# Optimization experiments

Hardware: AMD Instinct MI355X
Metric: run time of the kernel (lower is better)

Reference implementation:

```python
import jax, jax.numpy as jnp
import numpy as np

L, B, H, N2 = 2048, 16, 256, 32  # seq len, batch, d_model, d_state/2 (conjugate pairs)
EPS = 1e-5


def setup_inputs() -> dict:
    key = jax.random.key(0)
    ks = jax.random.split(key, 12)
    rn = lambda k, s, sc=1.0: sc * jax.random.normal(k, s, jnp.float32)
    x = rn(ks[0], (L, B, H))
    # S4 (SSSD) parameterization
    log_dt = jnp.log(0.001) + jax.random.uniform(ks[1], (H,), jnp.float32) * (np.log(0.1) - np.log(0.001))
    w_log_real = jnp.full((H, N2), np.log(0.5), jnp.float32)
    w_imag = jnp.pi * jnp.broadcast_to(jnp.arange(N2, dtype=jnp.float32), (H, N2))
    P_re, P_im = rn(ks[2], (1, H, N2), 0.1), rn(ks[3], (1, H, N2), 0.1)   # rank-1 low-rank term
    B_re, B_im = rn(ks[4], (1, H, N2), 0.5), rn(ks[5], (1, H, N2), 0.5)
    C_re, C_im = rn(ks[6], (2, H, N2), 0.5), rn(ks[7], (2, H, N2), 0.5)   # 2 channels (bidirectional)
    D = rn(ks[8], (1, H))
    Wout = rn(ks[9], (2 * H, H), 1.0 / np.sqrt(H))  # output linear -> GLU
    bout = jnp.zeros((2 * H,), jnp.float32)
    gamma = jnp.ones((H,), jnp.float32)
    beta = jnp.zeros((H,), jnp.float32)
    return dict(x=x, log_dt=log_dt, w_log_real=w_log_real, w_imag=w_imag,
                P_re=P_re, P_im=P_im, B_re=B_re, B_im=B_im, C_re=C_re, C_im=C_im,
                D=D, Wout=Wout, bout=bout, gamma=gamma, beta=beta)


def _s4_layer(x, log_dt, w_log_real, w_imag, P_re, P_im, B_re, B_im, C_re, C_im,
              D, Wout, bout, gamma, beta):
    u = jnp.transpose(x, (1, 2, 0))  # (B, H, L)
    Lx = u.shape[-1]
    # ---- SSKernelNPLR kernel generation (Cauchy resolvent + rank-1 Woodbury) ----
    dt = jnp.exp(log_dt)                               # (H,)
    w = -jnp.exp(w_log_real) + 1j * w_imag             # (H, N2)
    Bc = B_re + 1j * B_im                              # (1, H, N2)
    Cc = C_re + 1j * C_im                              # (2, H, N2)
    Pc = P_re + 1j * P_im                              # (1, H, N2)
    Bt = jnp.concatenate([Bc, Pc], axis=0)             # (2, H, N2)
    Ct = jnp.concatenate([Cc, jnp.conj(Pc)], axis=0)   # (3, H, N2)
    Fh = Lx // 2 + 1
    omega = jnp.exp(-2j * jnp.pi * jnp.arange(Fh) / Lx).astype(jnp.complex64)
    z = 2.0 * (1.0 - omega) / (1.0 + omega)            # bilinear-transform nodes
    wd = w * dt[:, None].astype(w.dtype)               # dt folded into A
    v = Bt[:, None, :, :] * Ct[None, :, :, :]          # (2, 3, H, N2)
    inv1 = 1.0 / (z[None, :, None] - wd[:, None, :])                 # (H, Fh, N2)
    inv2 = 1.0 / (z[None, :, None] - jnp.conj(wd)[:, None, :])
    # cauchy with conjugate-pair symmetry
    r = jnp.einsum('abhn,hfn->abhf', v, inv1) + jnp.einsum('abhn,hfn->abhf', jnp.conj(v), inv2)
    r = r * dt[None, None, :, None].astype(r.dtype)    # (2, 3, H, Fh)
    # rank-1 Woodbury correction
    k_f = r[:-1, :-1] - r[:-1, -1:] * r[-1:, :-1] / (1.0 + r[-1:, -1:])  # (1, 2, H, Fh)
    k_f = k_f * 2.0 / (1.0 + omega)
    k = jnp.fft.irfft(k_f, n=Lx, axis=-1)[0]           # (2, H, L) real kernel, 2 = fwd/bwd
    # ---- bidirectional FFT convolution ----
    kk = jnp.pad(k[0], ((0, 0), (0, Lx))) + jnp.pad(k[1][:, ::-1], ((0, 0), (Lx, 0)))  # (H, 2L)
    kf = jnp.fft.rfft(kk, n=2 * Lx)                    # (H, L+1)
    uf = jnp.fft.rfft(u, n=2 * Lx)                     # (B, H, L+1)
    y = jnp.fft.irfft(uf * kf[None], n=2 * Lx)[..., :Lx]  # (B, H, L)
    y = y + u * D[0][None, :, None]                    # skip connection D
    y = jax.nn.gelu(y, approximate=False)
    y2 = jnp.einsum('dh,bhl->bdl', Wout, y) + bout[None, :, None]  # (B, 2H, L)
    y = y2[:, :H] * jax.nn.sigmoid(y2[:, H:])          # GLU over channel dim
    # ---- wrapper: residual + permute back + LayerNorm ----
    xo = jnp.transpose(y + u, (2, 0, 1))               # (L, B, H)
    mu = jnp.mean(xo, axis=-1, keepdims=True)
    var = jnp.mean(jnp.square(xo - mu), axis=-1, keepdims=True)
    return (xo - mu) * jax.lax.rsqrt(var + EPS) * gamma + beta


def reference(x, log_dt, w_log_real, w_imag, P_re, P_im, B_re, B_im, C_re, C_im,
              D, Wout, bout, gamma, beta):
    return _s4_layer(x, log_dt, w_log_real, w_imag, P_re, P_im, B_re, B_im,
                     C_re, C_im, D, Wout, bout, gamma, beta)
```

## Files before the change

kernel.cpp:

```cpp
#include <hip/hip_runtime.h>


#define PI_F 3.14159265358979323846f
#define LP(i) ((i) + ((i) >> 4))

typedef __attribute__((ext_vector_type(8))) short bf16x8;
typedef __attribute__((ext_vector_type(4))) float f32x4;

__device__ __forceinline__ float2 cmulf(float2 a, float2 b) {
    return make_float2(a.x*b.x - a.y*b.y, a.x*b.y + a.y*b.x);
}
__device__ __forceinline__ unsigned short f2bf(float f) {
    unsigned int u = __float_as_uint(f);
    u += 0x7fffu + ((u >> 16) & 1u);
    return (unsigned short)(u >> 16);
}

template<int SGN>
__device__ __forceinline__ void fft16(float2 v[16]) {
    float2 tsw;
#define SW(i,j) { tsw = v[i]; v[i] = v[j]; v[j] = tsw; }
    SW(1,8) SW(2,4) SW(3,12) SW(5,10) SW(7,14) SW(11,13)
#undef SW
    const float C8[8] = {1.f, 0.92387953251f, 0.70710678119f, 0.38268343236f,
                         0.f, -0.38268343236f, -0.70710678119f, -0.92387953251f};
    const float S8[8] = {0.f, 0.38268343236f, 0.70710678119f, 0.92387953251f,
                         1.f, 0.92387953251f, 0.70710678119f, 0.38268343236f};
    #pragma unroll
    for (int s = 0; s < 4; ++s) {
        const int Ns = 1 << s;
        #pragma unroll
        for (int j = 0; j < 8; ++j) {
            const int k  = j & (Ns - 1);
            const int i0 = ((j >> s) << (s + 1)) | k;
            const int i1 = i0 + Ns;
            const int ti = k << (3 - s);
            const float cs = C8[ti];
            const float sn = (SGN < 0) ? -S8[ti] : S8[ti];
            float2 a = v[i0], b = v[i1];
            float2 t = make_float2(cs*b.x - sn*b.y, cs*b.y + sn*b.x);
            v[i0] = make_float2(a.x + t.x, a.y + t.y);
            v[i1] = make_float2(a.x - t.x, a.y - t.y);
        }
    }
}

template<int SGN>
__device__ __forceinline__ void fft4096p(float2 v[16], float2* lds, int t) {
    fft16<SGN>(v);
    float s1, c1;
    __sincosf((float)SGN * (2.0f * PI_F / 4096.0f) * (float)t, &s1, &c1);
    float2 w1 = make_float2(c1, s1), cur = make_float2(1.f, 0.f);
    #pragma unroll
    for (int k = 1; k < 16; ++k) { cur = cmulf(cur, w1); v[k] = cmulf(v[k], cur); }
    __syncthreads();
    #pragma unroll
    for (int k = 0; k < 16; ++k) lds[t * 17 + k] = v[k];
    __syncthreads();
    const int k1 = t & 15, m2 = t >> 4;
    #pragma unroll
    for (int m1 = 0; m1 < 16; ++m1) v[m1] = lds[(m1 * 16 + m2) * 17 + k1];
    fft16<SGN>(v);
    float s2, c2;
    __sincosf((float)SGN * (2.0f * PI_F / 256.0f) * (float)m2, &s2, &c2);
    float2 w2 = make_float2(c2, s2); cur = make_float2(1.f, 0.f);
    #pragma unroll
    for (int j = 1; j < 16; ++j) { cur = cmulf(cur, w2); v[j] = cmulf(v[j], cur); }
    __syncthreads();
    #pragma unroll
    for (int j = 0; j < 16; ++j) lds[m2 * 273 + j * 17 + k1] = v[j];
    __syncthreads();
    #pragma unroll
    for (int m = 0; m < 16; ++m) v[m] = lds[m * 273 + (t >> 4) * 17 + k1];
    fft16<SGN>(v);
}

template<int SGN>
__device__ __forceinline__ void fft_fused(float2* A, int N, int logN,
                                          int tid, int nthr) {
    __syncthreads();
    for (int j = tid; j < N; j += nthr) {
        int r = (int)(__brev((unsigned)j) >> (32 - logN));
        if (r > j) { float2 t = A[LP(j)]; A[LP(j)] = A[LP(r)]; A[LP(r)] = t; }
    }
    __syncthreads();
    int s = 0;
    if (logN & 1) {
        for (int j = tid; j < (N >> 1); j += nthr) {
            int i0 = 2 * j;
            float2 a = A[LP(i0)], b = A[LP(i0 + 1)];
            A[LP(i0)]     = make_float2(a.x + b.x, a.y + b.y);
            A[LP(i0 + 1)] = make_float2(a.x - b.x, a.y - b.y);
        }
        __syncthreads();
        s = 1;
    }
    for (; s < logN; s += 2) {
        const int Ns = 1 << s;
        for (int g = tid; g < (N >> 2); g += nthr) {
            int k = g & (Ns - 1);
            int base = ((g >> s) << (s + 2)) | k;
            float2 a0 = A[LP(base)];
            float2 a1 = A[LP(base + Ns)];
            float2 a2 = A[LP(base + 2*Ns)];
            float2 a3 = A[LP(base + 3*Ns)];
            float ang1 = (float)SGN * PI_F * (float)k / (float)Ns;
            float sn1, cs1; __sincosf(ang1, &sn1, &cs1);
            float2 t = make_float2(cs1*a1.x - sn1*a1.y, cs1*a1.y + sn1*a1.x);
            float2 b0 = make_float2(a0.x + t.x, a0.y + t.y);
            float2 b1 = make_float2(a0.x - t.x, a0.y - t.y);
            t = make_float2(cs1*a3.x - sn1*a3.y, cs1*a3.y + sn1*a3.x);
            float2 b2 = make_float2(a2.x + t.x, a2.y + t.y);
            float2 b3 = make_float2(a2.x - t.x, a2.y - t.y);
            float ang2 = (float)SGN * PI_F * (float)k / (float)(2 * Ns);
            float sn2, cs2; __sincosf(ang2, &sn2, &cs2);
            t = make_float2(cs2*b2.x - sn2*b2.y, cs2*b2.y + sn2*b2.x);
            A[LP(base)]        = make_float2(b0.x + t.x, b0.y + t.y);
            A[LP(base + 2*Ns)] = make_float2(b0.x - t.x, b0.y - t.y);
            float c2p, s2p;
            if (SGN < 0) { c2p = sn2; s2p = -cs2; } else { c2p = -sn2; s2p = cs2; }
            t = make_float2(c2p*b3.x - s2p*b3.y, c2p*b3.y + s2p*b3.x);
            A[LP(base + Ns)]   = make_float2(b1.x + t.x, b1.y + t.y);
            A[LP(base + 3*Ns)] = make_float2(b1.x - t.x, b1.y - t.y);
        }
        __syncthreads();
    }
}

__global__ void k0_convW(const float* __restrict__ W, unsigned short* __restrict__ Wb)
{
    int i = blockIdx.x * 256 + threadIdx.x;
    if (i < 512 * 256) Wb[i] = f2bf(W[i]);
}

__global__ __launch_bounds__(256) void k1_kergen(const float* __restrict__ log_dt,
                          const float* __restrict__ wlr, const float* __restrict__ wim,
                          const float* __restrict__ Pre, const float* __restrict__ Pim,
                          const float* __restrict__ Bre, const float* __restrict__ Bim,
                          const float* __restrict__ Cre, const float* __restrict__ Cim,
                          float2* __restrict__ kf_out)
{
    __shared__ float4 T0[32], T1[32], T2[32], T3[32];
    int h = blockIdx.x;
    int tid = threadIdx.x;
    float dt = expf(log_dt[h]);
    if (tid < 32) {
        int i = h * 32 + tid;
        float wre = -expf(wlr[i]) * dt;
        float wi  = wim[i] * dt;
        float2 B  = make_float2(Bre[i], Bim[i]);
        float2 P  = make_float2(Pre[i], Pim[i]);
        float2 C0 = make_float2(Cre[i], Cim[i]);
        float2 C1 = make_float2(Cre[8192 + i], Cim[8192 + i]);
        float2 Pc = make_float2(P.x, -P.y);
        float2 v00 = cmulf(B, C0), v01 = cmulf(B, C1), v02 = cmulf(B, Pc);
        float2 v10 = cmulf(P, C0), v11 = cmulf(P, C1), v12 = cmulf(P, Pc);
        T0[tid] = make_float4(wre, wi, v00.x, v00.y);
        T1[tid] = make_float4(v01.x, v01.y, v02.x, v02.y);
        T2[tid] = make_float4(v10.x, v10.y, v11.x, v11.y);
        T3[tid] = make_float4(v12.x, v12.y, 0.f, 0.f);
    }
    __syncthreads();
    int f = blockIdx.y * 256 + tid;
    if (f > 1024) return;
    float ang = -(2.0f * PI_F / 2048.0f) * (float)f;
    float sn, cs;
    sincosf(ang, &sn, &cs);
    float2 onep = make_float2(1.0f + cs, sn);
    float invo = __builtin_amdgcn_rcpf(onep.x * onep.x + onep.y * onep.y);
    float2 oinv = make_float2(onep.x * invo, -onep.y * invo);
    float2 z = cmulf(make_float2(2.0f * (1.0f - cs), -2.0f * sn), oinv);
    float2 r00 = {0,0}, r01 = {0,0}, r02 = {0,0};
    float2 r10 = {0,0}, r11 = {0,0}, r12 = {0,0};
    #pragma unroll 4
    for (int n = 0; n < 32; ++n) {
        float4 a  = T0[n];
        float4 bq = T1[n];
        float4 cq = T2[n];
        float4 dq = T3[n];
        float zx  = z.x - a.x;
        float d1y = z.y - a.y;
        float d2y = z.y + a.y;
        float inv1 = __builtin_amdgcn_rcpf(zx * zx + d1y * d1y);
        float inv2 = __builtin_amdgcn_rcpf(zx * zx + d2y * d2y);
        float sx = zx * (inv1 + inv2);
        float dx = zx * (inv1 - inv2);
        float sy = -(d1y * inv1 + d2y * inv2);
        float dy = d1y * inv1 - d2y * inv2;
        r00.x += a.z*sx + a.w*dy;  r00.y += a.z*sy + a.w*dx;
        r01.x += bq.x*sx + bq.y*dy; r01.y += bq.x*sy + bq.y*dx;
        r02.x += bq.z*sx + bq.w*dy; r02.y += bq.z*sy + bq.w*dx;
        r10.x += cq.x*sx + cq.y*dy; r10.y += cq.x*sy + cq.y*dx;
        r11.x += cq.z*sx + cq.w*dy; r11.y += cq.z*sy + cq.w*dx;
        r12.x += dq.x*sx + dq.y*dy; r12.y += dq.x*sy + dq.y*dx;
    }
    r00.x *= dt; r00.y *= dt; r01.x *= dt; r01.y *= dt; r02.x *= dt; r02.y *= dt;
    r10.x *= dt; r10.y *= dt; r11.x *= dt; r11.y *= dt; r12.x *= dt; r12.y *= dt;
    float2 den = make_float2(1.0f + r12.x, r12.y);
    float invd = __builtin_amdgcn_rcpf(den.x * den.x + den.y * den.y);
    float2 idn = make_float2(den.x * invd, -den.y * invd);
    float2 fac = make_float2(2.0f * oinv.x, 2.0f * oinv.y);
    float2 t0 = cmulf(cmulf(r02, r10), idn);
    float2 k0 = cmulf(make_float2(r00.x - t0.x, r00.y - t0.y), fac);
    float2 t1 = cmulf(cmulf(r02, r11), idn);
    float2 k1 = cmulf(make_float2(r01.x - t1.x, r01.y - t1.y), fac);
    kf_out[(size_t)h * 1025 + f]         = k0;
    kf_out[(size_t)(256 + h) * 1025 + f] = k1;
}

__global__ __launch_bounds__(256) void k2_kernelfft(const float2* __restrict__ kfin,
                                                    float2* __restrict__ kfout)
{
    __shared__ float2 A2[2176];
    __shared__ float2 A4[4352];
    int h = blockIdx.x, tid = threadIdx.x;
    const float2* s0 = kfin + (size_t)h * 1025;
    const float2* s1 = kfin + (size_t)(256 + h) * 1025;
    for (int j = tid; j < 2048; j += 256) {
        float2 q0, q1;
        if (j == 0)          { q0 = s0[0];    q0.y = 0.0f; q1 = s1[0];    q1.y = 0.0f; }
        else if (j < 1024)   { q0 = s0[j];                 q1 = s1[j]; }
        else if (j == 1024)  { q0 = s0[1024]; q0.y = 0.0f; q1 = s1[1024]; q1.y = 0.0f; }
        else { float2 t0 = s0[2048 - j], t1 = s1[2048 - j];
               q0 = make_float2(t0.x, -t0.y); q1 = make_float2(t1.x, -t1.y); }
        A2[LP(j)] = make_float2(q0.x - q1.y, q0.y + q1.x);
    }
    fft_fused<+1>(A2, 2048, 11, tid, 256);
    const float scl = 1.0f / 2048.0f;
    for (int j = tid; j < 2048; j += 256) {
        float2 v = A2[LP(j)];
        A4[LP(j)]        = make_float2(v.x * scl, 0.0f);
        A4[LP(4095 - j)] = make_float2(v.y * scl, 0.0f);
    }
    fft_fused<-1>(A4, 4096, 12, tid, 256);
    for (int F = tid; F <= 2048; F += 256)
        kfout[(size_t)h * 2049 + F] = A4[LP(F)];
}

__global__ void k3_transpose(const float* __restrict__ x, float* __restrict__ u)
{
    __shared__ float tile[32][33];
    int p0 = blockIdx.x * 32;
    int l0 = blockIdx.y * 32;
    int tx = threadIdx.x, ty = threadIdx.y;
    for (int i = ty; i < 32; i += 8)
        tile[i][tx] = x[(size_t)(l0 + i) * 4096 + p0 + tx];
    __syncthreads();
    for (int i = ty; i < 32; i += 8)
        u[(size_t)(p0 + i) * 2048 + l0 + tx] = tile[tx][i];
}

__global__ __launch_bounds__(256) void k4_conv(const float* __restrict__ u,
        const float2* __restrict__ kf, const float* __restrict__ Dp,
        unsigned short* __restrict__ ygb)
{
    __shared__ float2 lds[4366];
    int h  = blockIdx.x & 255;
    int bp = blockIdx.x >> 8;
    int t  = threadIdx.x;
    const float* u0 = u + (size_t)((2*bp)   * 256 + h) * 2048;
    const float* u1 = u + (size_t)((2*bp+1) * 256 + h) * 2048;
    float2 v[16], us[8];
    #pragma unroll
    for (int n1 = 0; n1 < 8; ++n1) {
        int j = n1 * 256 + t;
        us[n1] = make_float2(u0[j], u1[j]);
        v[n1] = us[n1];
        v[n1 + 8] = make_float2(0.f, 0.f);
    }
    fft4096p<-1>(v, lds, t);
    const float2* kfh = kf + (size_t)h * 2049;
    #pragma unroll
    for (int j2 = 0; j2 < 16; ++j2) {
        int f = t + 256 * j2;
        float2 K;
        if (f <= 2048) K = kfh[f];
        else { float2 q = kfh[4096 - f]; K = make_float2(q.x, -q.y); }
        v[j2] = cmulf(v[j2], K);
    }
    fft4096p<+1>(v, lds, t);
    float d = Dp[h];
    unsigned short* o0 = ygb + (size_t)((2*bp)   * 256 + h) * 2048;
    unsigned short* o1 = ygb + (size_t)((2*bp+1) * 256 + h) * 2048;
    const float iscl = 1.0f / 4096.0f;
    #pragma unroll
    for (int j2 = 0; j2 < 8; ++j2) {
        int l = t + 256 * j2;
        float y0 = v[j2].x * iscl + d * us[j2].x;
        float y1 = v[j2].y * iscl + d * us[j2].y;
        o0[l] = f2bf(0.5f * y0 * (1.0f + erff(y0 * 0.70710678118654752f)));
        o1[l] = f2bf(0.5f * y1 * (1.0f + erff(y1 * 0.70710678118654752f)));
    }
}

__global__ __launch_bounds__(256, 2) void k56_gemm_glu_ln(const unsigned short* __restrict__ ygb,
        const unsigned short* __restrict__ Wb, const float* __restrict__ bout,
        const float* __restrict__ u, const float* __restrict__ gamma,
        const float* __restrict__ beta, float* __restrict__ out)
{
    __shared__ short yt[64][264];
    __shared__ short Wl[64][264];
    __shared__ float bo[512];
    __shared__ float gb2[512];
    int b  = blockIdx.y;
    int l0 = blockIdx.x * 64;
    int tid = threadIdx.x;
    int lane = tid & 63, w = tid >> 6;
    int cc = lane & 15, gg = lane >> 4;
    bo[tid] = bout[tid]; bo[tid + 256] = bout[tid + 256];
    gb2[tid] = gamma[tid]; gb2[tid + 256] = beta[tid];
    int li = tid & 63;
    #pragma unroll 4
    for (int it = 0; it < 64; ++it) {
        int hh = (tid >> 6) + it * 4;
        yt[li][hh] = (short)ygb[(size_t)(b * 256 + hh) * 2048 + l0 + li];
    }
    __syncthreads();
    const short* brow = &yt[16 * w + cc][0];
    bf16x8 bfr[8];
    #pragma unroll
    for (int ks = 0; ks < 8; ++ks) bfr[ks] = *(const bf16x8*)(brow + ks * 32 + gg * 8);
    f32x4 acc[32];
    #pragma unroll
    for (int tt = 0; tt < 32; ++tt) acc[tt] = (f32x4){0.f, 0.f, 0.f, 0.f};
    const int fr = tid >> 5, fch = tid & 31;
    bf16x8 pre[8];
    #pragma unroll
    for (int j = 0; j < 8; ++j)
        pre[j] = *(const bf16x8*)(Wb + (size_t)(fr + j * 8) * 256 + fch * 8);
    #pragma unroll
    for (int c = 0; c < 8; ++c) {
        #pragma unroll
        for (int j = 0; j < 8; ++j)
            *(bf16x8*)&Wl[fr + j * 8][fch * 8] = pre[j];
        __syncthreads();
        if (c < 7) {
            #pragma unroll
            for (int j = 0; j < 8; ++j)
                pre[j] = *(const bf16x8*)(Wb + (size_t)((c + 1) * 64 + fr + j * 8) * 256 + fch * 8);
        }
        #pragma unroll
        for (int ks = 0; ks < 8; ++ks) {
            #pragma unroll
            for (int tl = 0; tl < 4; ++tl) {
                bf16x8 afrag = *(const bf16x8*)&Wl[tl * 16 + cc][ks * 32 + gg * 8];
                acc[c * 4 + tl] = __builtin_amdgcn_mfma_f32_16x16x32_bf16(
                    afrag, bfr[ks], acc[c * 4 + tl], 0, 0, 0);
            }
        }
        __syncthreads();
    }
    int l = l0 + 16 * w + cc;
    const float* up = u + (size_t)b * 256 * 2048 + l;
    float s = 0.f, q2 = 0.f;
    #pragma unroll
    for (int tt = 0; tt < 16; ++tt) {
        #pragma unroll
        for (int r = 0; r < 4; ++r) {
            int P = tt * 16 + gg * 4 + r;
            float ya = acc[tt][r] + bo[P];
            float gb = acc[tt + 16][r] + bo[256 + P];
            float gv = ya / (1.0f + expf(-gb));
            float val = gv + up[(size_t)P * 2048];
            acc[tt][r] = val;
            s += val; q2 += val * val;
        }
    }
    s  += __shfl_xor(s, 16);  s  += __shfl_xor(s, 32);
    q2 += __shfl_xor(q2, 16); q2 += __shfl_xor(q2, 32);
    float mu = s * (1.0f / 256.0f);
    float var = q2 * (1.0f / 256.0f) - mu * mu;
    float rstd = rsqrtf(var + 1e-5f);
    float* ob = out + (size_t)(l * 16 + b) * 256;
    #pragma unroll
    for (int tt = 0; tt < 16; ++tt) {
        int P0 = tt * 16 + gg * 4;
        float4 o4;
        o4.x = (acc[tt][0] - mu) * rstd * gb2[P0 + 0] + gb2[256 + P0 + 0];
        o4.y = (acc[tt][1] - mu) * rstd * gb2[P0 + 1] + gb2[256 + P0 + 1];
        o4.z = (acc[tt][2] - mu) * rstd * gb2[P0 + 2] + gb2[256 + P0 + 2];
        o4.w = (acc[tt][3] - mu) * rstd * gb2[P0 + 3] + gb2[256 + P0 + 3];
        *(float4*)(ob + P0) = o4;
    }
}

extern "C" void kernel_launch(void* const* d_in, const int* in_sizes, int n_in,
                              void* d_out, int out_size, void* d_ws, size_t ws_size,
                              hipStream_t stream)
{
    (void)in_sizes; (void)n_in; (void)out_size; (void)ws_size;
    const float* x      = (const float*)d_in[0];
    const float* log_dt = (const float*)d_in[1];
    const float* wlr    = (const float*)d_in[2];
    const float* wim    = (const float*)d_in[3];
    const float* Pre    = (const float*)d_in[4];
    const float* Pim    = (const float*)d_in[5];
    const float* Bre    = (const float*)d_in[6];
    const float* Bim    = (const float*)d_in[7];
    const float* Cre    = (const float*)d_in[8];
    const float* Cim    = (const float*)d_in[9];
    const float* Dp     = (const float*)d_in[10];
    const float* Wout   = (const float*)d_in[11];
    const float* bout   = (const float*)d_in[12];
    const float* gamma  = (const float*)d_in[13];
    const float* beta   = (const float*)d_in[14];

    float* ws  = (float*)d_ws;
    float* u   = ws;
    unsigned short* ygb = (unsigned short*)(ws + 8388608);
    char*  ob  = (char*)d_out;
    float2* kF  = (float2*)(ob);
    float2* kfo = (float2*)(ob + 4198400);
    unsigned short* Wb = (unsigned short*)(ob + 8394752);

    k0_convW<<<dim3(512), 256, 0, stream>>>(Wout, Wb);
    k1_kergen<<<dim3(256, 5), 256, 0, stream>>>(log_dt, wlr, wim, Pre, Pim, Bre, Bim, Cre, Cim, kF);
    k2_kernelfft<<<dim3(256), 256, 0, stream>>>(kF, kfo);
    k3_transpose<<<dim3(128, 64), dim3(32, 8), 0, stream>>>(x, u);
    k4_conv<<<dim3(2048), 256, 0, stream>>>(u, kfo, Dp, ygb);
    k56_gemm_glu_ln<<<dim3(32, 16), 256, 0, stream>>>(ygb, Wb, bout, u, gamma, beta, (float*)d_out);
}
```

Before: 130.7 us.

## Widen kernel-FFT blocks, raise conv occupancy, stage residual in LDS for GLU+LN

Launches the kernel-FFT stage with 1024 threads per block instead of 256, adds a min-blocks hint of 4 to the conv kernel's launch bounds, and in the GEMM/GLU/LayerNorm kernel loads the residual tile into shared memory (aliasing the yt/Wl buffers) with coalesced reads. Before, each thread read the residual with a stride of 2048 floats. The changes target latency in the small-grid FFT and uncoalesced global reads in the epilogue. The occupancy hint may force register spills in the conv kernel, and the extra LDS pass adds a sync.

```diff
diff --git a/kernel.cpp b/kernel.cpp
--- a/kernel.cpp
+++ b/kernel.cpp
@@ -208,15 +208,16 @@
     kf_out[(size_t)(256 + h) * 1025 + f] = k1;
 }
 
-__global__ __launch_bounds__(256) void k2_kernelfft(const float2* __restrict__ kfin,
-                                                    float2* __restrict__ kfout)
+__global__ __launch_bounds__(1024) void k2_kernelfft(const float2* __restrict__ kfin,
+                                                     float2* __restrict__ kfout)
 {
     __shared__ float2 A2[2176];
     __shared__ float2 A4[4352];
     int h = blockIdx.x, tid = threadIdx.x;
+    const int NT = 1024;
     const float2* s0 = kfin + (size_t)h * 1025;
     const float2* s1 = kfin + (size_t)(256 + h) * 1025;
-    for (int j = tid; j < 2048; j += 256) {
+    for (int j = tid; j < 2048; j += NT) {
         float2 q0, q1;
         if (j == 0)          { q0 = s0[0];    q0.y = 0.0f; q1 = s1[0];    q1.y = 0.0f; }
         else if (j < 1024)   { q0 = s0[j];                 q1 = s1[j]; }
@@ -225,15 +226,15 @@
                q0 = make_float2(t0.x, -t0.y); q1 = make_float2(t1.x, -t1.y); }
         A2[LP(j)] = make_float2(q0.x - q1.y, q0.y + q1.x);
     }
-    fft_fused<+1>(A2, 2048, 11, tid, 256);
+    fft_fused<+1>(A2, 2048, 11, tid, NT);
     const float scl = 1.0f / 2048.0f;
-    for (int j = tid; j < 2048; j += 256) {
+    for (int j = tid; j < 2048; j += NT) {
         float2 v = A2[LP(j)];
         A4[LP(j)]        = make_float2(v.x * scl, 0.0f);
         A4[LP(4095 - j)] = make_float2(v.y * scl, 0.0f);
     }
-    fft_fused<-1>(A4, 4096, 12, tid, 256);
-    for (int F = tid; F <= 2048; F += 256)
+    fft_fused<-1>(A4, 4096, 12, tid, NT);
+    for (int F = tid; F <= 2048; F += NT)
         kfout[(size_t)h * 2049 + F] = A4[LP(F)];
 }
 
@@ -250,7 +251,7 @@
         u[(size_t)(p0 + i) * 2048 + l0 + tx] = tile[tx][i];
 }
 
-__global__ __launch_bounds__(256) void k4_conv(const float* __restrict__ u,
+__global__ __launch_bounds__(256, 4) void k4_conv(const float* __restrict__ u,
         const float2* __restrict__ kf, const float* __restrict__ Dp,
         unsigned short* __restrict__ ygb)
 {
@@ -298,8 +299,10 @@
         const float* __restrict__ u, const float* __restrict__ gamma,
         const float* __restrict__ beta, float* __restrict__ out)
 {
-    __shared__ short yt[64][264];
-    __shared__ short Wl[64][264];
+    __shared__ __align__(16) char smem[67584];
+    short (*yt)[264] = (short(*)[264])smem;
+    short (*Wl)[264] = (short(*)[264])(smem + 33792);
+    float (*uS)[65]  = (float(*)[65])smem;
     __shared__ float bo[512];
     __shared__ float gb2[512];
     int b  = blockIdx.y;
@@ -350,8 +353,12 @@
         }
         __syncthreads();
     }
-    int l = l0 + 16 * w + cc;
-    const float* up = u + (size_t)b * 256 * 2048 + l;
+    for (int i = tid; i < 256 * 64; i += 256) {
+        int hh = i >> 6, l = i & 63;
+        uS[hh][l] = u[(size_t)(b * 256 + hh) * 2048 + l0 + l];
+    }
+    __syncthreads();
+    int llocal = 16 * w + cc;
     float s = 0.f, q2 = 0.f;
     #pragma unroll
     for (int tt = 0; tt < 16; ++tt) {
@@ -361,7 +368,7 @@
             float ya = acc[tt][r] + bo[P];
             float gb = acc[tt + 16][r] + bo[256 + P];
             float gv = ya / (1.0f + expf(-gb));
-            float val = gv + up[(size_t)P * 2048];
+            float val = gv + uS[P][llocal];
             acc[tt][r] = val;
             s += val; q2 += val * val;
         }
@@ -371,7 +378,7 @@
     float mu = s * (1.0f / 256.0f);
     float var = q2 * (1.0f / 256.0f) - mu * mu;
     float rstd = rsqrtf(var + 1e-5f);
-    float* ob = out + (size_t)(l * 16 + b) * 256;
+    float* ob = out + (size_t)((l0 + llocal) * 16 + b) * 256;
     #pragma unroll
     for (int tt = 0; tt < 16; ++tt) {
         int P0 = tt * 16 + gg * 4;
@@ -415,7 +422,7 @@
 
     k0_convW<<<dim3(512), 256, 0, stream>>>(Wout, Wb);
     k1_kergen<<<dim3(256, 5), 256, 0, stream>>>(log_dt, wlr, wim, Pre, Pim, Bre, Bim, Cre, Cim, kF);
-    k2_kernelfft<<<dim3(256), 256, 0, stream>>>(kF, kfo);
+    k2_kernelfft<<<dim3(256), 1024, 0, stream>>>(kF, kfo);
     k3_transpose<<<dim3(128, 64), dim3(32, 8), 0, stream>>>(x, u);
     k4_conv<<<dim3(2048), 256, 0, stream>>>(u, kfo, Dp, ygb);
     k56_gemm_glu_ln<<<dim3(32, 16), 256, 0, stream>>>(ygb, Wb, bout, u, gamma, beta, (float*)d_out);
```

Measured after the change: 137.7 us. +5.4%, slower.
